# Kernel tuning notes

Measured on AMD Instinct MI355X. Metric: run time of the kernel, lower is better.

Reference implementation:

```python
import jax, jax.numpy as jnp
import numpy as np

N = 100000      # nodes
E = 1600000     # edges
NG = 512        # graphs in batch
FIN = 7         # in_features
HID = 128       # hidden_channels
OUT = 2         # outfeatures


def setup_inputs() -> dict:
    key = jax.random.key(0)
    ks = jax.random.split(key, 16)
    x = jax.random.normal(ks[0], (N, FIN), jnp.float32)
    edge_index = jax.random.randint(ks[1], (2, E), 0, N, dtype=jnp.int64)
    batch = jnp.sort(jax.random.randint(ks[2], (N,), 0, NG, dtype=jnp.int64))

    def lin_w(k, fan_in, fan_out):
        # glorot-ish init, scale irrelevant for correctness baseline
        return jax.random.normal(k, (fan_in, fan_out), jnp.float32) / np.sqrt(fan_in).astype(np.float32)

    W1 = lin_w(ks[3], FIN, HID); b1 = jnp.zeros((HID,), jnp.float32)
    W2 = lin_w(ks[4], HID, HID); b2 = jnp.zeros((HID,), jnp.float32)
    W3 = lin_w(ks[5], HID, HID); b3 = jnp.zeros((HID,), jnp.float32)
    W4 = lin_w(ks[6], HID, HID); b4 = jnp.zeros((HID,), jnp.float32)
    Wlin = lin_w(ks[7], HID, OUT); blin = jnp.zeros((OUT,), jnp.float32)
    return dict(x=x, edge_index=edge_index, batch=batch,
                W1=W1, b1=b1, W2=W2, b2=b2, W3=W3, b3=b3, W4=W4, b4=b4,
                Wlin=Wlin, blin=blin)


def gcn_conv(h, W, b, src, dst, n):
    # PyG GCNConv: h' = D^{-1/2} (A + I) D^{-1/2} (h W) + b
    # src/dst already include self-loops
    h = h @ W
    deg = jax.ops.segment_sum(jnp.ones(src.shape[0], h.dtype), dst, num_segments=n)
    dinv = jnp.where(deg > 0, jax.lax.rsqrt(deg), jnp.zeros_like(deg))
    norm = dinv[src] * dinv[dst]                       # [E+N]
    agg = jax.ops.segment_sum(norm[:, None] * h[src], dst, num_segments=n)
    return agg + b


def reference(x, edge_index, batch, W1, b1, W2, b2, W3, b3, W4, b4, Wlin, blin):
    loop = jnp.arange(N, dtype=edge_index.dtype)
    src = jnp.concatenate([edge_index[0], loop])       # add self-loops
    dst = jnp.concatenate([edge_index[1], loop])

    h = gcn_conv(x, W1, b1, src, dst, N)
    for W, b in ((W2, b2), (W3, b3), (W4, b4)):
        h = jax.nn.relu(h)
        h = gcn_conv(h, W, b, src, dst, N)

    # global mean pool per graph
    sums = jax.ops.segment_sum(h, batch, num_segments=NG)
    cnt = jax.ops.segment_sum(jnp.ones((N,), h.dtype), batch, num_segments=NG)
    pooled = sums / jnp.maximum(cnt, 1.0)[:, None]     # [NG, HID]

    # dropout is identity in eval mode
    return pooled @ Wlin + blin                        # [NG, OUT]
```

## Files before the change

kernel.cpp:

```cpp
#include <hip/hip_runtime.h>
#include <hip/hip_bf16.h>

#define N_NODES 100000
#define E_EDGES 1600000
#define NG 512
#define FIN 7
#define HID 128
#define NBUCK 782
#define NBLK_SC 256
#define CHUNK 6250
#define TLEN (NBUCK * NBLK_SC)
#define NCH 196
#define MMX_GRID 782
#define AGG4_GRID 6250

typedef __attribute__((ext_vector_type(8))) short bf16x8;
typedef __attribute__((ext_vector_type(4))) float f32x4;

__device__ __forceinline__ float bf_lo(unsigned int u) { return __uint_as_float(u << 16); }
__device__ __forceinline__ float bf_hi(unsigned int u) { return __uint_as_float(u & 0xffff0000u); }
__device__ __forceinline__ unsigned int f2bf_rne(float f) {
    unsigned int x = __float_as_uint(f);
    return (x + 0x7fffu + ((x >> 16) & 1u)) >> 16;
}
__device__ __forceinline__ unsigned int pack_bf2(float lo, float hi) {
    return f2bf_rne(lo) | (f2bf_rne(hi) << 16);
}


__global__ __launch_bounds__(256) void k_hist2(const int* __restrict__ eidx,
                                               int* __restrict__ table,
                                               const float* __restrict__ W4,
                                               const float* __restrict__ b4,
                                               const float* __restrict__ Wlin,
                                               const float* __restrict__ blin,
                                               float* __restrict__ Wc,
                                               float* __restrict__ bc,
                                               float* __restrict__ pooled,
                                               const float* __restrict__ W2,
                                               const float* __restrict__ W3,
                                               unsigned short* __restrict__ WT2,
                                               unsigned short* __restrict__ WT3) {
    __shared__ int h[NBUCK];
    int blk = blockIdx.x, t = threadIdx.x;
    if (blk >= NBLK_SC) {
        int r = blk - NBLK_SC;
        if (r < 64) {
            float4 z = {0.f, 0.f, 0.f, 0.f};
            *(float4*)&pooled[(r * 256 + t) * 4] = z;
        } else if (r == 64) {
            int k = t >> 1, o = t & 1;
            float acc = 0.f;
            for (int j = 0; j < HID; ++j) acc += W4[k * HID + j] * Wlin[j * 2 + o];
            Wc[k * 2 + o] = acc;
            if (k == 0) {
                float b = blin[o];
                for (int j = 0; j < HID; ++j) b += b4[j] * Wlin[j * 2 + o];
                bc[o] = b;
            }
        } else if (r < 129) {
            int idx = (r - 65) * 256 + t;
            int k = idx >> 7, n = idx & 127;
            WT2[n * 128 + k] = (unsigned short)f2bf_rne(W2[idx]);
        } else {
            int idx = (r - 129) * 256 + t;
            int k = idx >> 7, n = idx & 127;
            WT3[n * 128 + k] = (unsigned short)f2bf_rne(W3[idx]);
        }
        return;
    }
    for (int i = t; i < NBUCK; i += 256) h[i] = 0;
    __syncthreads();
    int e0 = blk * CHUNK, e1 = e0 + CHUNK;
    for (int e = e0 + t; e < e1; e += 256)
        atomicAdd(&h[eidx[E_EDGES + e] >> 7], 1);
    __syncthreads();
    for (int i = t; i < NBUCK; i += 256)
        table[i * NBLK_SC + blk] = h[i];
}

__global__ void k_blocksum(const int* __restrict__ table, int* __restrict__ partial) {
    __shared__ int s[256];
    int b = blockIdx.x, t = threadIdx.x;
    int base = b * 1024;
    int sum = 0;
    for (int i = t; i < 1024; i += 256) {
        int idx = base + i;
        sum += (idx < TLEN) ? table[idx] : 0;
    }
    s[t] = sum; __syncthreads();
    for (int st = 128; st > 0; st >>= 1) {
        if (t < st) s[t] += s[t + st];
        __syncthreads();
    }
    if (t == 0) partial[b] = s[0];
}

__global__ void k_scan_blk(int* __restrict__ partial, int* __restrict__ bucketBase,
                           int* __restrict__ rowptr) {
    __shared__ int s[256];
    int t = threadIdx.x;
    int v = (t < NCH) ? partial[t] : 0;
    s[t] = v; __syncthreads();
    for (int st = 1; st < 256; st <<= 1) {
        int a = (t >= st) ? s[t - st] : 0;
        __syncthreads();
        s[t] += a;
        __syncthreads();
    }
    if (t < NCH) partial[t] = s[t] - v;
    if (t == 0) { bucketBase[NBUCK] = E_EDGES; rowptr[N_NODES] = E_EDGES; }
}

__global__ void k_scan_final(int* __restrict__ table, const int* __restrict__ partial,
                             int* __restrict__ bucketBase) {
    __shared__ int s[1024];
    int b = blockIdx.x, t = threadIdx.x;
    int idx = b * 1024 + t;
    int v = (idx < TLEN) ? table[idx] : 0;
    s[t] = v; __syncthreads();
    for (int st = 1; st < 1024; st <<= 1) {
        int add = (t >= st) ? s[t - st] : 0;
        __syncthreads();
        s[t] += add;
        __syncthreads();
    }
    if (idx < TLEN) {
        int ex = partial[b] + s[t] - v;
        table[idx] = ex;
        if ((idx & (NBLK_SC - 1)) == 0) bucketBase[idx / NBLK_SC] = ex;
    }
}

__global__ __launch_bounds__(256) void k_scatter2(const int* __restrict__ eidx,
                                                  const int* __restrict__ table,
                                                  unsigned int* __restrict__ ebuf) {
    __shared__ int loff[NBUCK];
    int blk = blockIdx.x, t = threadIdx.x;
    for (int i = t; i < NBUCK; i += 256) loff[i] = table[i * NBLK_SC + blk];
    __syncthreads();
    int e0 = blk * CHUNK, e1 = e0 + CHUNK;
    for (int e = e0 + t; e < e1; e += 256) {
        int s = eidx[e];
        int d = eidx[E_EDGES + e];
        int p = atomicAdd(&loff[d >> 7], 1);
        ebuf[p] = ((unsigned int)(d & 127) << 17) | (unsigned int)s;
    }
}

__global__ __launch_bounds__(256) void k_bucket(const unsigned int* __restrict__ ebuf,
                                                const int* __restrict__ bucketBase,
                                                int* __restrict__ rowptr,
                                                float* __restrict__ dinv,
                                                int* __restrict__ col) {
    __shared__ int scnt[128], soff[128], scur[128];
    int b = blockIdx.x, t = threadIdx.x;
    int bbase = bucketBase[b], bend = bucketBase[b + 1];
    if (t < 128) { scnt[t] = 0; scur[t] = 0; }
    __syncthreads();
    for (int e = bbase + t; e < bend; e += 256) {
        unsigned int rec = ebuf[e];
        atomicAdd(&scnt[rec >> 17], 1);
    }
    __syncthreads();
    if (t < 128) soff[t] = scnt[t];
    __syncthreads();
    for (int st = 1; st < 128; st <<= 1) {
        int a = (t < 128 && t >= st) ? soff[t - st] : 0;
        __syncthreads();
        if (t < 128) soff[t] += a;
        __syncthreads();
    }
    if (t < 128) {
        int ex = soff[t] - scnt[t];
        int node = b * 128 + t;
        if (node < N_NODES) {
            rowptr[node] = bbase + ex;
            dinv[node] = rsqrtf((float)(scnt[t] + 1));
        }
        soff[t] = ex;
    }
    __syncthreads();
    for (int e = bbase + t; e < bend; e += 256) {
        unsigned int rec = ebuf[e];
        int dl = rec >> 17;
        int s = rec & 0x1FFFF;
        int p = bbase + soff[dl] + atomicAdd(&scur[dl], 1);
        col[p] = (dl << 20) | s;
    }
}


__global__ __launch_bounds__(256) void k_l1(const float* __restrict__ x,
                                            const float* __restrict__ W1,
                                            const float* __restrict__ b1,
                                            const int* __restrict__ rowptr,
                                            const int* __restrict__ col,
                                            const float* __restrict__ dinv,
                                            unsigned int* __restrict__ g1) {
    __shared__ float axs[32][8];
    __shared__ float w1s[FIN * HID];
    __shared__ float b1s[HID];
    int t = threadIdx.x;
    for (int i = t; i < FIN * HID; i += 256) w1s[i] = W1[i];
    if (t < HID) b1s[t] = b1[t];

    int lane = t & 63, wave = t >> 6;
    int sub = lane >> 3, f = lane & 7;
    int node = blockIdx.x * 32 + wave * 8 + sub;
    bool valid = node < N_NODES;
    float di = valid ? dinv[node] : 0.f;
    float a = (valid && f < 7) ? di * x[node * FIN + f] : 0.f;
    int e0 = valid ? rowptr[node] : 0;
    int e1 = valid ? rowptr[node + 1] : 0;
    for (int base = e0; base < e1; base += 8) {
        int mm = e1 - base; if (mm > 8) mm = 8;
        int sc = (f < mm) ? (col[base + f] & 0x1FFFF) : 0;
        for (int j = 0; j < mm; ++j) {
            int s = __shfl(sc, sub * 8 + j);
            float v = (f < 7) ? x[s * FIN + f] : dinv[s];
            float ds = __shfl(v, sub * 8 + 7);
            if (f < 7) a += ds * v;
        }
    }
    axs[wave * 8 + sub][f] = (f < 7) ? di * a : 0.f;
    __syncthreads();

    int nl = t >> 3, fb = t & 7;
    int gnode = blockIdx.x * 32 + nl;
    if (gnode < N_NODES) {
        float av[FIN];
        #pragma unroll
        for (int k = 0; k < FIN; ++k) av[k] = axs[nl][k];
        float dsc = dinv[gnode];
        unsigned int outp[8];
        #pragma unroll
        for (int p = 0; p < 8; ++p) {
            int fo = fb * 16 + p * 2;
            float acc0 = b1s[fo], acc1 = b1s[fo + 1];
            #pragma unroll
            for (int k = 0; k < FIN; ++k) {
                acc0 += av[k] * w1s[k * HID + fo];
                acc1 += av[k] * w1s[k * HID + fo + 1];
            }
            outp[p] = pack_bf2(dsc * fmaxf(acc0, 0.f), dsc * fmaxf(acc1, 0.f));
        }
        *(uint4*)&g1[(size_t)gnode * 64 + fb * 8] = *(uint4*)&outp[0];
        *(uint4*)&g1[(size_t)gnode * 64 + fb * 8 + 4] = *(uint4*)&outp[4];
    }
}


__global__ __launch_bounds__(256) void k_agg4(const unsigned int* __restrict__ gIn,
                                              unsigned int* __restrict__ gOut,
                                              const int* __restrict__ rowptr,
                                              const int* __restrict__ colv,
                                              const float* __restrict__ dinv) {
    int wid = (blockIdx.x * blockDim.x + threadIdx.x) >> 6;
    int lane = threadIdx.x & 63;
    int q = lane >> 4, r = lane & 15;
    int node = wid * 4 + q;
    if (node >= N_NODES) return;

    const uint4* grow = (const uint4*)gIn;
    float di = dinv[node];

    uint4 su = grow[(size_t)node * 16 + r];
    float a0 = bf_lo(su.x), a1 = bf_hi(su.x);
    float a2 = bf_lo(su.y), a3 = bf_hi(su.y);
    float a4 = bf_lo(su.z), a5 = bf_hi(su.z);
    float a6 = bf_lo(su.w), a7 = bf_hi(su.w);

    int e0 = rowptr[node];
    int e1 = rowptr[node + 1];
    for (int base = e0; base < e1; base += 16) {
        int m = e1 - base; if (m > 16) m = 16;
        int cv = (r < m) ? colv[base + r] : 0;
        uint4 u[16];
        #pragma unroll
        for (int j = 0; j < 16; ++j) {
            if (j < m) {
                int s = __shfl(cv, q * 16 + j) & 0x1FFFF;
                u[j] = grow[(size_t)s * 16 + r];
            }
        }
        #pragma unroll
        for (int j = 0; j < 16; ++j) {
            if (j < m) {
                a0 += bf_lo(u[j].x); a1 += bf_hi(u[j].x);
                a2 += bf_lo(u[j].y); a3 += bf_hi(u[j].y);
                a4 += bf_lo(u[j].z); a5 += bf_hi(u[j].z);
                a6 += bf_lo(u[j].w); a7 += bf_hi(u[j].w);
            }
        }
    }

    uint4 o;
    o.x = pack_bf2(di * a0, di * a1);
    o.y = pack_bf2(di * a2, di * a3);
    o.z = pack_bf2(di * a4, di * a5);
    o.w = pack_bf2(di * a6, di * a7);
    *(uint4*)&gOut[(size_t)node * 64 + r * 4] = o;
}


__global__ __launch_bounds__(256) void k_mmx(const unsigned int* __restrict__ gIn,
                                             const unsigned short* __restrict__ WTg,
                                             const float* __restrict__ bias,
                                             const float* __restrict__ dinv,
                                             unsigned int* __restrict__ outg) {
    __shared__ unsigned short sbuf[128 * 136];
    int t = threadIdx.x;
    for (int i = t * 8; i < 128 * 128; i += 256 * 8) {
        int n = i >> 7, k = i & 127;
        uint4 val = *(const uint4*)(WTg + i);
        *(uint4*)(sbuf + n * 136 + k) = val;
    }

    int lane = t & 63, wave = t >> 6;
    int m = lane & 15, quad = lane >> 4;
    int nodeBase = blockIdx.x * 128 + wave * 32;
    const short* gs = (const short*)gIn;

    float bi[8];
    #pragma unroll
    for (int nt = 0; nt < 8; ++nt) bi[nt] = bias[nt * 16 + m];

    f32x4 acc[2][8];
    #pragma unroll
    for (int gi = 0; gi < 2; ++gi)
        #pragma unroll
        for (int nt = 0; nt < 8; ++nt)
            acc[gi][nt] = (f32x4){0.f, 0.f, 0.f, 0.f};

    __syncthreads();

    #pragma unroll
    for (int kc = 0; kc < 4; ++kc) {
        bf16x8 ah[2];
        #pragma unroll
        for (int gi = 0; gi < 2; ++gi) {
            int node = nodeBase + gi * 16 + m;
            bf16x8 h = {0, 0, 0, 0, 0, 0, 0, 0};
            if (node < N_NODES)
                h = *(const bf16x8*)(gs + (size_t)node * 128 + kc * 32 + quad * 8);
            ah[gi] = h;
        }
        #pragma unroll
        for (int nt = 0; nt < 8; ++nt) {
            bf16x8 b = *(const bf16x8*)(sbuf + (nt * 16 + m) * 136 + kc * 32 + quad * 8);
            #pragma unroll
            for (int gi = 0; gi < 2; ++gi)
                acc[gi][nt] = __builtin_amdgcn_mfma_f32_16x16x32_bf16(ah[gi], b, acc[gi][nt], 0, 0, 0);
        }
    }

    __syncthreads();
    #pragma unroll
    for (int gi = 0; gi < 2; ++gi)
        #pragma unroll
        for (int r = 0; r < 4; ++r) {
            int nl = wave * 32 + gi * 16 + quad * 4 + r;
            int node = blockIdx.x * 128 + nl;
            float di = (node < N_NODES) ? dinv[node] : 0.f;
            #pragma unroll
            for (int nt = 0; nt < 8; ++nt) {
                float vv = acc[gi][nt][r] + bi[nt];
                sbuf[nl * 132 + nt * 16 + m] = (unsigned short)f2bf_rne(di * fmaxf(vv, 0.f));
            }
        }
    __syncthreads();
    for (int i = t; i < 128 * 32; i += 256) {
        int nl = i >> 5, p = i & 31;
        int node = blockIdx.x * 128 + nl;
        if (node < N_NODES) {
            uint2 val = *(const uint2*)(sbuf + nl * 132 + p * 4);
            *(uint2*)&outg[(size_t)node * 64 + p * 2] = val;
        }
    }
}


__global__ __launch_bounds__(256) void k_poolsum(const unsigned int* __restrict__ aggB,
                                                 const int* __restrict__ batch,
                                                 float* __restrict__ pooled) {
    int wid = (blockIdx.x * blockDim.x + threadIdx.x) >> 6;
    int lane = threadIdx.x & 63;
    int n0 = wid * 16;
    if (n0 >= N_NODES) return;
    int n1 = n0 + 16; if (n1 > N_NODES) n1 = N_NODES;
    int curg = batch[n0];
    float ax = 0.f, ay = 0.f;
    for (int n = n0; n < n1; ++n) {
        int g = batch[n];
        if (g != curg) {
            atomicAdd(&pooled[curg * HID + 2 * lane], ax);
            atomicAdd(&pooled[curg * HID + 2 * lane + 1], ay);
            ax = 0.f; ay = 0.f; curg = g;
        }
        unsigned int u = aggB[(size_t)n * 64 + lane];
        ax += bf_lo(u); ay += bf_hi(u);
    }
    atomicAdd(&pooled[curg * HID + 2 * lane], ax);
    atomicAdd(&pooled[curg * HID + 2 * lane + 1], ay);
}


__global__ void k_head(const float* __restrict__ pooled, const int* __restrict__ batch,
                       const float* __restrict__ Wc, const float* __restrict__ bc,
                       const float* __restrict__ blin, float* __restrict__ out) {
    int wid = (blockIdx.x * blockDim.x + threadIdx.x) >> 6;
    int lane = threadIdx.x & 63;
    if (wid >= NG) return;
    int g = wid;
    int lo = 0, hi = N_NODES;
    while (lo < hi) { int mid = (lo + hi) >> 1; if (batch[mid] < g) lo = mid + 1; else hi = mid; }
    int start = lo;
    hi = N_NODES;
    while (lo < hi) { int mid = (lo + hi) >> 1; if (batch[mid] < g + 1) lo = mid + 1; else hi = mid; }
    int cnt = lo - start;
    float invc = (cnt > 0) ? 1.0f / (float)cnt : 0.f;
    float px = pooled[g * HID + 2 * lane] * invc;
    float py = pooled[g * HID + 2 * lane + 1] * invc;

    #pragma unroll
    for (int o = 0; o < 2; ++o) {
        float v = px * Wc[(2 * lane) * 2 + o] + py * Wc[(2 * lane + 1) * 2 + o];
        #pragma unroll
        for (int s = 32; s > 0; s >>= 1) v += __shfl_down(v, s);
        if (lane == 0) out[g * 2 + o] = (cnt > 0) ? (v + bc[o]) : blin[o];
    }
}


extern "C" void kernel_launch(void* const* d_in, const int* in_sizes, int n_in,
                              void* d_out, int out_size, void* d_ws, size_t ws_size,
                              hipStream_t stream) {
    const float* x    = (const float*)d_in[0];
    const int*   eidx = (const int*)d_in[1];
    const int*   batch= (const int*)d_in[2];
    const float* W1   = (const float*)d_in[3];
    const float* b1   = (const float*)d_in[4];
    const float* W2   = (const float*)d_in[5];
    const float* b2   = (const float*)d_in[6];
    const float* W3   = (const float*)d_in[7];
    const float* b3   = (const float*)d_in[8];
    const float* W4   = (const float*)d_in[9];
    const float* b4   = (const float*)d_in[10];
    const float* Wlin = (const float*)d_in[11];
    const float* blin = (const float*)d_in[12];
    float* out = (float*)d_out;

    char* ws = (char*)d_ws;
    size_t off = 0;
    auto carve = [&](size_t bytes) { char* p = ws + off; off = (off + bytes + 255) & ~(size_t)255; return p; };
    int*   rowptr    = (int*)carve((size_t)(N_NODES + 1) * 4);
    float* dinv      = (float*)carve((size_t)N_NODES * 4);
    int*   col       = (int*)carve((size_t)E_EDGES * 4);
    unsigned int* ebuf = (unsigned int*)carve((size_t)E_EDGES * 4);
    int*   table     = (int*)carve((size_t)TLEN * 4);
    int*   partial   = (int*)carve((size_t)NCH * 4);
    int*   bucketBase= (int*)carve((size_t)(NBUCK + 1) * 4);
    unsigned int* gA = (unsigned int*)carve((size_t)N_NODES * 64 * 4);
    unsigned int* gB = (unsigned int*)carve((size_t)N_NODES * 64 * 4);
    float* pooled    = (float*)carve((size_t)NG * HID * 4);
    float* Wc        = (float*)carve((size_t)HID * 2 * 4);
    float* bc        = (float*)carve(2 * 4);
    unsigned short* WT2 = (unsigned short*)carve((size_t)HID * HID * 2);
    unsigned short* WT3 = (unsigned short*)carve((size_t)HID * HID * 2);
    (void)ws_size; (void)n_in; (void)in_sizes; (void)out_size;

    const int BLK = 256;
    int gridL1 = (N_NODES + 31) / 32;
    int gridPS = ((N_NODES + 15) / 16 * 64 + BLK - 1) / BLK;
    int gridHead = (NG * 64 + BLK - 1) / BLK;

    k_hist2<<<NBLK_SC + 193, BLK, 0, stream>>>(eidx, table, W4, b4, Wlin, blin,
                                               Wc, bc, pooled, W2, W3, WT2, WT3);
    k_blocksum<<<NCH, BLK, 0, stream>>>(table, partial);
    k_scan_blk<<<1, 256, 0, stream>>>(partial, bucketBase, rowptr);
    k_scan_final<<<NCH, 1024, 0, stream>>>(table, partial, bucketBase);
    k_scatter2<<<NBLK_SC, BLK, 0, stream>>>(eidx, table, ebuf);
    k_bucket<<<NBUCK, BLK, 0, stream>>>(ebuf, bucketBase, rowptr, dinv, col);

    k_l1<<<gridL1, BLK, 0, stream>>>(x, W1, b1, rowptr, col, dinv, gA);

    k_agg4<<<AGG4_GRID, BLK, 0, stream>>>(gA, gB, rowptr, col, dinv);
    k_mmx<<<MMX_GRID, BLK, 0, stream>>>(gB, WT2, b2, dinv, gA);
    k_agg4<<<AGG4_GRID, BLK, 0, stream>>>(gA, gB, rowptr, col, dinv);
    k_mmx<<<MMX_GRID, BLK, 0, stream>>>(gB, WT3, b3, dinv, gA);
    k_agg4<<<AGG4_GRID, BLK, 0, stream>>>(gA, gB, rowptr, col, dinv);

    k_poolsum<<<gridPS, BLK, 0, stream>>>(gB, batch, pooled);
    k_head<<<gridHead, BLK, 0, stream>>>(pooled, batch, Wc, bc, blin, out);
}
```

Measured before the change: 433.1 us.

## Aggregate with one wavefront per node and prefetch neighbor indices

The SpMM aggregation kernel changes from four nodes per wavefront (16 lanes each loading uint4) to one node per wavefront, with each lane loading one 32-bit bf16 pair per neighbor row. Column indices are loaded 64 at a time, and the next batch is prefetched while gathers run in unrolled groups of 8 and 4. The col array now stores plain source indices, so the masking disappears. The aim is to raise wavefront count and memory-level parallelism, at the cost of narrower per-lane loads, more shuffles, and lanes left idle on low-degree nodes.

Measured after the change: 407.8 us. 1.06x faster.

```diff
diff --git a/kernel.cpp b/kernel.cpp
--- a/kernel.cpp
+++ b/kernel.cpp
@@ -12,7 +12,7 @@
 #define TLEN (NBUCK * NBLK_SC)
 #define NCH 196
 #define MMX_GRID 782
-#define AGG4_GRID 6250
+#define AGGW_GRID 25000
 
 typedef __attribute__((ext_vector_type(8))) short bf16x8;
 typedef __attribute__((ext_vector_type(4))) float f32x4;
@@ -186,7 +186,7 @@
         int dl = rec >> 17;
         int s = rec & 0x1FFFF;
         int p = bbase + soff[dl] + atomicAdd(&scur[dl], 1);
-        col[p] = (dl << 20) | s;
+        col[p] = s;
     }
 }
 
@@ -215,7 +215,7 @@
     int e1 = valid ? rowptr[node + 1] : 0;
     for (int base = e0; base < e1; base += 8) {
         int mm = e1 - base; if (mm > 8) mm = 8;
-        int sc = (f < mm) ? (col[base + f] & 0x1FFFF) : 0;
+        int sc = (f < mm) ? col[base + f] : 0;
         for (int j = 0; j < mm; ++j) {
             int s = __shfl(sc, sub * 8 + j);
             float v = (f < 7) ? x[s * FIN + f] : dinv[s];
@@ -251,56 +251,68 @@
 }
 
 
-__global__ __launch_bounds__(256) void k_agg4(const unsigned int* __restrict__ gIn,
+__global__ __launch_bounds__(256) void k_aggW(const unsigned int* __restrict__ gIn,
                                               unsigned int* __restrict__ gOut,
                                               const int* __restrict__ rowptr,
                                               const int* __restrict__ colv,
                                               const float* __restrict__ dinv) {
     int wid = (blockIdx.x * blockDim.x + threadIdx.x) >> 6;
     int lane = threadIdx.x & 63;
-    int q = lane >> 4, r = lane & 15;
-    int node = wid * 4 + q;
-    if (node >= N_NODES) return;
-
-    const uint4* grow = (const uint4*)gIn;
-    float di = dinv[node];
-
-    uint4 su = grow[(size_t)node * 16 + r];
-    float a0 = bf_lo(su.x), a1 = bf_hi(su.x);
-    float a2 = bf_lo(su.y), a3 = bf_hi(su.y);
-    float a4 = bf_lo(su.z), a5 = bf_hi(su.z);
-    float a6 = bf_lo(su.w), a7 = bf_hi(su.w);
-
-    int e0 = rowptr[node];
-    int e1 = rowptr[node + 1];
-    for (int base = e0; base < e1; base += 16) {
-        int m = e1 - base; if (m > 16) m = 16;
-        int cv = (r < m) ? colv[base + r] : 0;
-        uint4 u[16];
-        #pragma unroll
-        for (int j = 0; j < 16; ++j) {
-            if (j < m) {
-                int s = __shfl(cv, q * 16 + j) & 0x1FFFF;
-                u[j] = grow[(size_t)s * 16 + r];
-            }
-        }
-        #pragma unroll
-        for (int j = 0; j < 16; ++j) {
-            if (j < m) {
-                a0 += bf_lo(u[j].x); a1 += bf_hi(u[j].x);
-                a2 += bf_lo(u[j].y); a3 += bf_hi(u[j].y);
-                a4 += bf_lo(u[j].z); a5 += bf_hi(u[j].z);
-                a6 += bf_lo(u[j].w); a7 += bf_hi(u[j].w);
-            }
-        }
-    }
-
-    uint4 o;
-    o.x = pack_bf2(di * a0, di * a1);
-    o.y = pack_bf2(di * a2, di * a3);
-    o.z = pack_bf2(di * a4, di * a5);
-    o.w = pack_bf2(di * a6, di * a7);
-    *(uint4*)&gOut[(size_t)node * 64 + r * 4] = o;
+    if (wid >= N_NODES) return;
+    int i = wid;
+    float di = dinv[i];
+    int e0 = rowptr[i], e1 = rowptr[i + 1];
+    int cv = colv[e0 + lane];
+    unsigned int v = gIn[(size_t)i * 64 + lane];
+    float ax = bf_lo(v), ay = bf_hi(v);
+
+    for (int base = e0; base < e1; base += 64) {
+        int m = e1 - base; if (m > 64) m = 64;
+        int cvn = cv;
+        if (base + 64 < e1) cvn = colv[base + 64 + lane];
+        int j = 0;
+        for (; j + 7 < m; j += 8) {
+            int s0 = __shfl(cv, j),     s1 = __shfl(cv, j + 1);
+            int s2 = __shfl(cv, j + 2), s3 = __shfl(cv, j + 3);
+            int s4 = __shfl(cv, j + 4), s5 = __shfl(cv, j + 5);
+            int s6 = __shfl(cv, j + 6), s7 = __shfl(cv, j + 7);
+            unsigned int u0 = gIn[(size_t)s0 * 64 + lane];
+            unsigned int u1 = gIn[(size_t)s1 * 64 + lane];
+            unsigned int u2 = gIn[(size_t)s2 * 64 + lane];
+            unsigned int u3 = gIn[(size_t)s3 * 64 + lane];
+            unsigned int u4 = gIn[(size_t)s4 * 64 + lane];
+            unsigned int u5 = gIn[(size_t)s5 * 64 + lane];
+            unsigned int u6 = gIn[(size_t)s6 * 64 + lane];
+            unsigned int u7 = gIn[(size_t)s7 * 64 + lane];
+            ax += bf_lo(u0); ay += bf_hi(u0);
+            ax += bf_lo(u1); ay += bf_hi(u1);
+            ax += bf_lo(u2); ay += bf_hi(u2);
+            ax += bf_lo(u3); ay += bf_hi(u3);
+            ax += bf_lo(u4); ay += bf_hi(u4);
+            ax += bf_lo(u5); ay += bf_hi(u5);
+            ax += bf_lo(u6); ay += bf_hi(u6);
+            ax += bf_lo(u7); ay += bf_hi(u7);
+        }
+        for (; j + 3 < m; j += 4) {
+            int s0 = __shfl(cv, j),     s1 = __shfl(cv, j + 1);
+            int s2 = __shfl(cv, j + 2), s3 = __shfl(cv, j + 3);
+            unsigned int u0 = gIn[(size_t)s0 * 64 + lane];
+            unsigned int u1 = gIn[(size_t)s1 * 64 + lane];
+            unsigned int u2 = gIn[(size_t)s2 * 64 + lane];
+            unsigned int u3 = gIn[(size_t)s3 * 64 + lane];
+            ax += bf_lo(u0); ay += bf_hi(u0);
+            ax += bf_lo(u1); ay += bf_hi(u1);
+            ax += bf_lo(u2); ay += bf_hi(u2);
+            ax += bf_lo(u3); ay += bf_hi(u3);
+        }
+        for (; j < m; ++j) {
+            int s0 = __shfl(cv, j);
+            unsigned int u0 = gIn[(size_t)s0 * 64 + lane];
+            ax += bf_lo(u0); ay += bf_hi(u0);
+        }
+        cv = cvn;
+    }
+    gOut[(size_t)i * 64 + lane] = pack_bf2(di * ax, di * ay);
 }
 
 
@@ -485,11 +497,11 @@
 
     k_l1<<<gridL1, BLK, 0, stream>>>(x, W1, b1, rowptr, col, dinv, gA);
 
-    k_agg4<<<AGG4_GRID, BLK, 0, stream>>>(gA, gB, rowptr, col, dinv);
+    k_aggW<<<AGGW_GRID, BLK, 0, stream>>>(gA, gB, rowptr, col, dinv);
     k_mmx<<<MMX_GRID, BLK, 0, stream>>>(gB, WT2, b2, dinv, gA);
-    k_agg4<<<AGG4_GRID, BLK, 0, stream>>>(gA, gB, rowptr, col, dinv);
+    k_aggW<<<AGGW_GRID, BLK, 0, stream>>>(gA, gB, rowptr, col, dinv);
     k_mmx<<<MMX_GRID, BLK, 0, stream>>>(gB, WT3, b3, dinv, gA);
-    k_agg4<<<AGG4_GRID, BLK, 0, stream>>>(gA, gB, rowptr, col, dinv);
+    k_aggW<<<AGGW_GRID, BLK, 0, stream>>>(gA, gB, rowptr, col, dinv);
 
     k_poolsum<<<gridPS, BLK, 0, stream>>>(gB, batch, pooled);
     k_head<<<gridHead, BLK, 0, stream>>>(pooled, batch, Wc, bc, blin, out);
```
